# Optimization experiments

Hardware: AMD Instinct MI355X
Metric: run time of the kernel (lower is better)

## Reference

```python
import jax, jax.numpy as jnp
import numpy as np
import math

B, C, A, W, H = 8, 128, 16, 64, 64


def setup_inputs() -> dict:
    key = jax.random.key(0)
    ks = jax.random.split(key, 7)
    s_in = 1.0 / math.sqrt(C)
    return {
        "x": jax.random.normal(ks[0], (B, C, W, H), dtype=jnp.float32),
        "Wq": jax.random.normal(ks[1], (A, C), dtype=jnp.float32) * s_in,
        "bq": jnp.zeros((A,), dtype=jnp.float32),
        "Wk": jax.random.normal(ks[2], (A, C), dtype=jnp.float32) * s_in,
        "bk": jnp.zeros((A,), dtype=jnp.float32),
        "Wv": jax.random.normal(ks[3], (C, C), dtype=jnp.float32) * s_in,
        "bv": jnp.zeros((C,), dtype=jnp.float32),
    }


def reference(x, Wq, bq, Wk, bk, Wv, bv):
    # 1x1 convs == per-pixel linear projections
    q = jnp.einsum('ac,bcwh->bawh', Wq, x) + bq[None, :, None, None]  # [B,A,W,H]
    k = jnp.einsum('ac,bcwh->bawh', Wk, x) + bk[None, :, None, None]  # [B,A,W,H]
    v = jnp.einsum('vc,bcwh->bvwh', Wv, x) + bv[None, :, None, None]  # [B,C,W,H]

    scale = 1.0 / math.sqrt(q.shape[1])
    # full spatial attention: [B, W, H, W, H]
    attn = jnp.einsum('bawh,baWH->bwhWH', q, k)
    b, w, h, _, _ = attn.shape
    attn = jax.nn.softmax(attn.reshape(b, w, h, -1) * scale, axis=-1)
    attn = attn.reshape(b, w, h, w, h)
    out = jnp.einsum('bwhWH,bvWH->bvwh', attn, v)  # [B,C,W,H]
    return out
```

## Files before the change

### kernel.cpp

```cpp
#include <hip/hip_runtime.h>
#include <math.h>

#define BB 8
#define CC 128
#define NN 4096

typedef _Float16 f16;
typedef _Float16 f16x4v __attribute__((ext_vector_type(4)));
typedef _Float16 f16x8 __attribute__((ext_vector_type(8)));
typedef float f32x4v __attribute__((ext_vector_type(4)));
typedef float f32x16 __attribute__((ext_vector_type(16)));

#if __has_builtin(__builtin_amdgcn_exp2f)
#define EXP2(x) __builtin_amdgcn_exp2f(x)
#else
#define EXP2(x) __expf((x)*0.69314718056f)
#endif

#define QSCALE 0.360673760222f
#define SHIFT  5.770780163555f

#define WF_BYTES 65536

__global__ __launch_bounds__(256)
void prep_kernel(const float* __restrict__ Wq, const float* __restrict__ bq,
                 const float* __restrict__ Wk, const float* __restrict__ bk,
                 const float* __restrict__ Wv, const float* __restrict__ bv,
                 f16* __restrict__ Wf, float* __restrict__ biasS)
{
    const int tg = blockIdx.x*256 + threadIdx.x;
    if (tg < 2560) {
        const int mt = tg >> 9, ks = (tg >> 6) & 7, l = tg & 63;
        const int n32 = l & 31, h = l >> 5;
        const int r = mt*32 + n32;
        f16x8 v8;
        #pragma unroll
        for (int i = 0; i < 8; i++) {
            int c = ks*16 + 8*h + i;
            float wv_;
            if (r < 16)      wv_ = QSCALE * Wq[r*CC + c];
            else if (r < 32) wv_ = Wk[(r-16)*CC + c];
            else             wv_ = Wv[(r-32)*CC + c];
            v8[i] = (f16)wv_;
        }
        *(f16x8*)&Wf[(size_t)tg*8] = v8;
    }
    if (blockIdx.x == 0 && threadIdx.x < 160) {
        int r = threadIdx.x;
        biasS[r] = r < 16 ? QSCALE*bq[r] : (r < 32 ? bk[r-16] : bv[r-32]);
    }
}

__global__ __launch_bounds__(256)
void proj_kernel(const float* __restrict__ x, const f16* __restrict__ Wf,
                 const float* __restrict__ biasS,
                 f16* __restrict__ Qt, f16* __restrict__ Kt, f16* __restrict__ Vf)
{
    __shared__ __align__(16) f16 Vl[CC*140];

    const int tid  = threadIdx.x;
    const int lane = tid & 63;
    const int wv   = tid >> 6;
    const int b    = blockIdx.x & 7;
    const int pt   = blockIdx.x >> 3;
    const int n32  = lane & 31;
    const int half = lane >> 5;
    const int p    = pt*128 + wv*32 + n32;

    const float* xp = x + (size_t)b*CC*NN + p;
    f16x8 xf[8];
    #pragma unroll
    for (int ks = 0; ks < 8; ks++) {
        float xv[8];
        #pragma unroll
        for (int i = 0; i < 8; i++)
            xv[i] = __builtin_nontemporal_load(&xp[(size_t)(ks*16 + 8*half + i)*NN]);
        #pragma unroll
        for (int i = 0; i < 8; i++) xf[ks][i] = (f16)xv[i];
    }

    f32x16 acc[5];
    #pragma unroll
    for (int mt = 0; mt < 5; mt++) acc[mt] = (f32x16)0.0f;
    #pragma unroll
    for (int ks = 0; ks < 8; ks++) {
        #pragma unroll
        for (int mt = 0; mt < 5; mt++) {
            f16x8 wfr = *(const f16x8*)&Wf[((size_t)(mt*8 + ks)*64 + lane)*8];
            acc[mt] = __builtin_amdgcn_mfma_f32_32x32x16_f16(wfr, xf[ks], acc[mt], 0, 0, 0);
        }
    }

    #pragma unroll
    for (int mt = 0; mt < 5; mt++) {
        #pragma unroll
        for (int q = 0; q < 4; q++) {
            float4 b4 = *(const float4*)&biasS[mt*32 + q*8 + 4*half];
            acc[mt][q*4+0] += b4.x; acc[mt][q*4+1] += b4.y;
            acc[mt][q*4+2] += b4.z; acc[mt][q*4+3] += b4.w;
        }
    }

    {
        size_t qkoff = ((size_t)b*NN + p)*16;
        f16x4v s0, s1, s2, s3;
        #pragma unroll
        for (int i = 0; i < 4; i++) {
            s0[i] = (f16)acc[0][i];    s1[i] = (f16)acc[0][4+i];
            s2[i] = (f16)acc[0][8+i];  s3[i] = (f16)acc[0][12+i];
        }
        *(f16x4v*)&Qt[qkoff + 4*half]     = s0;
        *(f16x4v*)&Qt[qkoff + 8 + 4*half] = s1;
        *(f16x4v*)&Kt[qkoff + 4*half]     = s2;
        *(f16x4v*)&Kt[qkoff + 8 + 4*half] = s3;
    }

    #pragma unroll
    for (int mt = 1; mt < 5; mt++) {
        #pragma unroll
        for (int g = 0; g < 16; g++) {
            int c = (mt-1)*32 + (g & 3) + 8*(g >> 2) + 4*half;
            Vl[c*140 + wv*32 + n32] = (f16)acc[mt][g];
        }
    }
    __syncthreads();

    #pragma unroll
    for (int pass = 0; pass < 8; pass++) {
        int item = pass*256 + tid;
        int l    = item & 63;
        int f    = (item >> 6) & 15;
        int ktl  = item >> 10;
        int c16  = f >> 2, ct = f & 3;
        int li   = l & 31, h2 = l >> 5;
        const f16* src = &Vl[(ct*32 + li)*140 + ktl*64 + c16*16 + 4*h2];
        f16x4v lo = *(const f16x4v*)&src[0];
        f16x4v hi = *(const f16x4v*)&src[8];
        f16x8 v8;
        #pragma unroll
        for (int i = 0; i < 4; i++) { v8[i] = lo[i]; v8[4+i] = hi[i]; }
        int ktg = pt*2 + ktl;
        *(f16x8*)&Vf[((((size_t)b*64 + ktg)*16 + c16*4 + ct)*64 + l)*8] = v8;
    }
}

__global__ __launch_bounds__(256, 2)
void attn_kernel(const f16* __restrict__ Qt, const f16* __restrict__ Kt,
                 const f16* __restrict__ Vf, float* __restrict__ out)
{
    __shared__ __align__(16) unsigned char lds_raw[53504];

    const int tid  = threadIdx.x;
    const int lane = tid & 63;
    const int w    = tid >> 6;
    const int cp   = w & 1;
    const int kh   = w >> 1;
    const int b    = blockIdx.x & 7;
    const int qt   = blockIdx.x >> 3;
    const int q0   = qt*64;
    const int n32  = lane & 31;
    const int half = lane >> 5;

    const f16* vb = Vf + (size_t)b*64*16*512;
    const f16* kb = Kt + (size_t)b*NN*16;
    const f16x8 qf = *(const f16x8*)&Qt[((size_t)b*NN + q0 + cp*32 + n32)*16 + half*8];

    f32x16 ofA[2], ofB[2];
    #pragma unroll
    for (int c = 0; c < 2; c++) { ofA[c] = (f32x16)0.0f; ofB[c] = (f32x16)0.0f; }
    float ps[4] = {0.f, 0.f, 0.f, 0.f};

    f16x8 kf0 = *(const f16x8*)&kb[((size_t)kh*64 + n32)*16 + half*8];
    f16x8 kf1 = *(const f16x8*)&kb[((size_t)kh*64 + 32 + n32)*16 + half*8];
    f16x8 vpf[8];
    {
        const f16* vt = vb + (size_t)kh*8192;
        #pragma unroll
        for (int kc = 0; kc < 4; kc++)
            #pragma unroll
            for (int j = 0; j < 2; j++)
                vpf[kc*2+j] = *(const f16x8*)&vt[((size_t)(kc*4 + 2*cp + j)*64 + lane)*8];
    }

    f16* Pex = (f16*)lds_raw;
    int pb = 0;

    for (int kt = kh; kt < NN/64; kt += 2) {
        const int ktn = (kt + 2 < NN/64) ? kt + 2 : kt;
        f16x8 kf0n = *(const f16x8*)&kb[((size_t)ktn*64 + n32)*16 + half*8];
        f16x8 kf1n = *(const f16x8*)&kb[((size_t)ktn*64 + 32 + n32)*16 + half*8];

        f16x8 po[4];
        {
            f32x16 St0 = __builtin_amdgcn_mfma_f32_32x32x16_f16(kf0, qf, (f32x16)(-SHIFT), 0, 0, 0);
            f32x16 St1 = __builtin_amdgcn_mfma_f32_32x32x16_f16(kf1, qf, (f32x16)(-SHIFT), 0, 0, 0);
            #pragma unroll
            for (int g = 0; g < 16; g++) {
                float e0 = EXP2(St0[g]); ps[g & 3] += e0; po[(g >> 3)][g & 7]     = (f16)e0;
                float e1 = EXP2(St1[g]); ps[g & 3] += e1; po[2 + (g >> 3)][g & 7] = (f16)e1;
            }
        }

        {
            f16* wr = &Pex[((size_t)(w*2 + pb)*4*64 + lane)*8];
            #pragma unroll
            for (int kc = 0; kc < 4; kc++)
                *(f16x8*)&wr[kc*512] = po[kc];
        }

        #pragma unroll
        for (int kc = 0; kc < 4; kc++) {
            #pragma unroll
            for (int j = 0; j < 2; j++) {
                if (cp == 0)
                    ofA[j] = __builtin_amdgcn_mfma_f32_32x32x16_f16(po[kc], vpf[kc*2+j], ofA[j], 0, 0, 0);
                else
                    ofB[j] = __builtin_amdgcn_mfma_f32_32x32x16_f16(po[kc], vpf[kc*2+j], ofB[j], 0, 0, 0);
            }
        }

        asm volatile("s_waitcnt lgkmcnt(0)\n\ts_barrier" ::: "memory");

        f16x8 pq[4];
        {
            const f16* rd = &Pex[((size_t)((w^1)*2 + pb)*4*64 + lane)*8];
            #pragma unroll
            for (int kc = 0; kc < 4; kc++)
                pq[kc] = *(const f16x8*)&rd[kc*512];
        }

        const f16* vtn = vb + (size_t)ktn*8192;
        #pragma unroll
        for (int kc = 0; kc < 4; kc++) {
            #pragma unroll
            for (int j = 0; j < 2; j++) {
                const int ii = kc*2 + j;
                f16x8 vc = vpf[ii];
                vpf[ii] = *(const f16x8*)&vtn[((size_t)(kc*4 + 2*cp + j)*64 + lane)*8];
                if (cp == 0)
                    ofB[j] = __builtin_amdgcn_mfma_f32_32x32x16_f16(pq[kc], vc, ofB[j], 0, 0, 0);
                else
                    ofA[j] = __builtin_amdgcn_mfma_f32_32x32x16_f16(pq[kc], vc, ofA[j], 0, 0, 0);
            }
        }

        kf0 = kf0n; kf1 = kf1n; pb ^= 1;
    }

    float ls = (ps[0] + ps[1]) + (ps[2] + ps[3]);
    ls += __shfl_xor(ls, 32);

    __syncthreads();
    if (w >= 2) {
        unsigned char* base = lds_raw + (size_t)cp*9216 + (size_t)lane*144;
        #pragma unroll
        for (int a = 0; a < 4; a++) {
            #pragma unroll
            for (int h = 0; h < 2; h++) {
                f16x8 t;
                #pragma unroll
                for (int jj = 0; jj < 8; jj++)
                    t[jj] = (f16)((a < 2 ? ofA[a & 1] : ofB[a & 1])[h*8 + jj]);
                *(f16x8*)(base + a*32 + h*16) = t;
            }
        }
        *(float*)(base + 128) = ls;
    }
    __syncthreads();
    if (w < 2) {
        unsigned char* base = lds_raw + (size_t)cp*9216 + (size_t)lane*144;
        #pragma unroll
        for (int a = 0; a < 4; a++) {
            #pragma unroll
            for (int h = 0; h < 2; h++) {
                f16x8 t = *(const f16x8*)(base + a*32 + h*16);
                #pragma unroll
                for (int jj = 0; jj < 8; jj++) {
                    float v = (float)t[jj];
                    if (a < 2) ofA[a & 1][h*8 + jj] += v;
                    else       ofB[a & 1][h*8 + jj] += v;
                }
            }
        }
        ls += *(const float*)(base + 128);
        float* ls_inv = (float*)(lds_raw + 18432);
        if (lane < 32) ls_inv[cp*32 + n32] = 1.f / ls;
    }
    __syncthreads();

    if (w < 2) {
        const float* ls_inv = (const float*)(lds_raw + 18432);
        float* Tb = (float*)(lds_raw + 18688);
        #pragma unroll
        for (int qts = 0; qts < 2; qts++) {
            #pragma unroll
            for (int j = 0; j < 4; j++) {
                f32x4v iv = *(const f32x4v*)&ls_inv[qts*32 + 8*j + 4*half];
                #pragma unroll
                for (int ctl = 0; ctl < 2; ctl++) {
                    const int c = (2*cp + ctl)*32 + n32;
                    f32x4v o;
                    #pragma unroll
                    for (int e = 0; e < 4; e++)
                        o[e] = (qts ? ofB[ctl] : ofA[ctl])[4*j + e] * iv[e];
                    *(f32x4v*)&Tb[(size_t)c*68 + qts*32 + 8*j + 4*half] = o;
                }
            }
        }
    }
    __syncthreads();
    {
        const float* Tb = (const float*)(lds_raw + 18688);
        #pragma unroll
        for (int it = 0; it < 8; it++) {
            int idx = it*256 + tid;
            int c = idx >> 4, qg = idx & 15;
            f32x4v v = *(const f32x4v*)&Tb[(size_t)c*68 + qg*4];
            __builtin_nontemporal_store(v,
                (f32x4v*)&out[((size_t)b*CC + c)*NN + q0 + qg*4]);
        }
    }
}

extern "C" void kernel_launch(void* const* d_in, const int* in_sizes, int n_in,
                              void* d_out, int out_size, void* d_ws, size_t ws_size,
                              hipStream_t stream) {
    const float* x  = (const float*)d_in[0];
    const float* Wq = (const float*)d_in[1];
    const float* bq = (const float*)d_in[2];
    const float* Wk = (const float*)d_in[3];
    const float* bk = (const float*)d_in[4];
    const float* Wv = (const float*)d_in[5];
    const float* bv = (const float*)d_in[6];
    float* out = (float*)d_out;

    f16* Qw = (f16*)d_ws;
    f16* Kw = Qw + (size_t)BB*NN*16;
    f16* Vw = Kw + (size_t)BB*NN*16;
    unsigned char* tail = (unsigned char*)d_out + (size_t)out_size*4 - WF_BYTES;
    f16*   Wf    = (f16*)tail;
    float* biasS = (float*)(tail + 49152);

    hipLaunchKernelGGL(prep_kernel, dim3(10), dim3(256), 0, stream,
                       Wq, bq, Wk, bk, Wv, bv, Wf, biasS);
    hipLaunchKernelGGL(proj_kernel, dim3(256), dim3(256), 0, stream,
                       x, Wf, biasS, Qw, Kw, Vw);
    hipLaunchKernelGGL(attn_kernel, dim3(512), dim3(256), 0, stream,
                       Qw, Kw, Vw, out);
}
```

Baseline: 136.9 us.

## Double-buffer K/V prefetch two tiles ahead and merge P·V MMAs after barrier

Keeps two register sets of K and V fragments so loads are issued two key tiles ahead, with the loop manually unrolled by two and an explicit epilogue. All P·V MMAs, for both the own and the exchanged probability tile, are moved after the LDS barrier. This hides global-load latency behind more compute at the cost of higher register pressure, which could lower occupancy or cause spills.

```diff
diff --git a/kernel.cpp b/kernel.cpp
--- a/kernel.cpp
+++ b/kernel.cpp
@@ -170,82 +170,115 @@
     for (int c = 0; c < 2; c++) { ofA[c] = (f32x16)0.0f; ofB[c] = (f32x16)0.0f; }
     float ps[4] = {0.f, 0.f, 0.f, 0.f};
 
-    f16x8 kf0 = *(const f16x8*)&kb[((size_t)kh*64 + n32)*16 + half*8];
-    f16x8 kf1 = *(const f16x8*)&kb[((size_t)kh*64 + 32 + n32)*16 + half*8];
-    f16x8 vpf[8];
+    f16x8 kfA0 = *(const f16x8*)&kb[((size_t)kh*64 + n32)*16 + half*8];
+    f16x8 kfA1 = *(const f16x8*)&kb[((size_t)kh*64 + 32 + n32)*16 + half*8];
+    f16x8 kfB0 = *(const f16x8*)&kb[((size_t)(kh+2)*64 + n32)*16 + half*8];
+    f16x8 kfB1 = *(const f16x8*)&kb[((size_t)(kh+2)*64 + 32 + n32)*16 + half*8];
+    f16x8 vpfA[8], vpfB[8];
     {
-        const f16* vt = vb + (size_t)kh*8192;
+        const f16* vtA = vb + (size_t)kh*8192;
+        const f16* vtB = vb + (size_t)(kh+2)*8192;
         #pragma unroll
         for (int kc = 0; kc < 4; kc++)
             #pragma unroll
-            for (int j = 0; j < 2; j++)
-                vpf[kc*2+j] = *(const f16x8*)&vt[((size_t)(kc*4 + 2*cp + j)*64 + lane)*8];
+            for (int j = 0; j < 2; j++) {
+                vpfA[kc*2+j] = *(const f16x8*)&vtA[((size_t)(kc*4 + 2*cp + j)*64 + lane)*8];
+                vpfB[kc*2+j] = *(const f16x8*)&vtB[((size_t)(kc*4 + 2*cp + j)*64 + lane)*8];
+            }
     }
 
     f16* Pex = (f16*)lds_raw;
     int pb = 0;
-
-    for (int kt = kh; kt < NN/64; kt += 2) {
-        const int ktn = (kt + 2 < NN/64) ? kt + 2 : kt;
-        f16x8 kf0n = *(const f16x8*)&kb[((size_t)ktn*64 + n32)*16 + half*8];
-        f16x8 kf1n = *(const f16x8*)&kb[((size_t)ktn*64 + 32 + n32)*16 + half*8];
-
+    const int klast = kh + 62;
+
+#define STEP(KT, KF0, KF1, VPF)                                                       \
+    {                                                                                 \
+        f32x16 St0 = __builtin_amdgcn_mfma_f32_32x32x16_f16(KF0, qf, (f32x16)(-SHIFT), 0, 0, 0); \
+        f32x16 St1 = __builtin_amdgcn_mfma_f32_32x32x16_f16(KF1, qf, (f32x16)(-SHIFT), 0, 0, 0); \
+        int tl = (KT) + 4; if (tl > klast) tl = (KT);                                 \
+        KF0 = *(const f16x8*)&kb[((size_t)tl*64 + n32)*16 + half*8];                  \
+        KF1 = *(const f16x8*)&kb[((size_t)tl*64 + 32 + n32)*16 + half*8];             \
+        f16x8 po[4];                                                                  \
+        _Pragma("unroll")                                                             \
+        for (int g = 0; g < 16; g++) {                                                \
+            float e0 = EXP2(St0[g]); ps[g & 3] += e0; po[(g >> 3)][g & 7]     = (f16)e0; \
+            float e1 = EXP2(St1[g]); ps[g & 3] += e1; po[2 + (g >> 3)][g & 7] = (f16)e1; \
+        }                                                                             \
+        {                                                                             \
+            f16* wr = &Pex[((size_t)(w*2 + pb)*4*64 + lane)*8];                       \
+            _Pragma("unroll")                                                         \
+            for (int kc = 0; kc < 4; kc++) *(f16x8*)&wr[kc*512] = po[kc];             \
+        }                                                                             \
+        asm volatile("s_waitcnt lgkmcnt(0)\n\ts_barrier" ::: "memory");               \
+        f16x8 pq[4];                                                                  \
+        {                                                                             \
+            const f16* rd = &Pex[((size_t)((w^1)*2 + pb)*4*64 + lane)*8];             \
+            _Pragma("unroll")                                                         \
+            for (int kc = 0; kc < 4; kc++) pq[kc] = *(const f16x8*)&rd[kc*512];       \
+        }                                                                             \
+        const f16* vtn = vb + (size_t)tl*8192;                                        \
+        _Pragma("unroll")                                                             \
+        for (int kc = 0; kc < 4; kc++) {                                              \
+            _Pragma("unroll")                                                         \
+            for (int j = 0; j < 2; j++) {                                             \
+                const int ii = kc*2 + j;                                              \
+                f16x8 vc = VPF[ii];                                                   \
+                VPF[ii] = *(const f16x8*)&vtn[((size_t)(kc*4 + 2*cp + j)*64 + lane)*8]; \
+                if (cp == 0) {                                                        \
+                    ofA[j] = __builtin_amdgcn_mfma_f32_32x32x16_f16(po[kc], vc, ofA[j], 0, 0, 0); \
+                    ofB[j] = __builtin_amdgcn_mfma_f32_32x32x16_f16(pq[kc], vc, ofB[j], 0, 0, 0); \
+                } else {                                                              \
+                    ofA[j] = __builtin_amdgcn_mfma_f32_32x32x16_f16(pq[kc], vc, ofA[j], 0, 0, 0); \
+                    ofB[j] = __builtin_amdgcn_mfma_f32_32x32x16_f16(po[kc], vc, ofB[j], 0, 0, 0); \
+                }                                                                     \
+            }                                                                         \
+        }                                                                             \
+        pb ^= 1;                                                                      \
+    }
+
+    for (int it = 0; it < 15; ++it) {
+        const int kt = kh + it*4;
+        STEP(kt,     kfA0, kfA1, vpfA)
+        STEP(kt + 2, kfB0, kfB1, vpfB)
+    }
+    STEP(kh + 60, kfA0, kfA1, vpfA)
+    {
+        f32x16 St0 = __builtin_amdgcn_mfma_f32_32x32x16_f16(kfB0, qf, (f32x16)(-SHIFT), 0, 0, 0);
+        f32x16 St1 = __builtin_amdgcn_mfma_f32_32x32x16_f16(kfB1, qf, (f32x16)(-SHIFT), 0, 0, 0);
         f16x8 po[4];
-        {
-            f32x16 St0 = __builtin_amdgcn_mfma_f32_32x32x16_f16(kf0, qf, (f32x16)(-SHIFT), 0, 0, 0);
-            f32x16 St1 = __builtin_amdgcn_mfma_f32_32x32x16_f16(kf1, qf, (f32x16)(-SHIFT), 0, 0, 0);
-            #pragma unroll
-            for (int g = 0; g < 16; g++) {
-                float e0 = EXP2(St0[g]); ps[g & 3] += e0; po[(g >> 3)][g & 7]     = (f16)e0;
-                float e1 = EXP2(St1[g]); ps[g & 3] += e1; po[2 + (g >> 3)][g & 7] = (f16)e1;
-            }
-        }
-
+        #pragma unroll
+        for (int g = 0; g < 16; g++) {
+            float e0 = EXP2(St0[g]); ps[g & 3] += e0; po[(g >> 3)][g & 7]     = (f16)e0;
+            float e1 = EXP2(St1[g]); ps[g & 3] += e1; po[2 + (g >> 3)][g & 7] = (f16)e1;
+        }
         {
             f16* wr = &Pex[((size_t)(w*2 + pb)*4*64 + lane)*8];
             #pragma unroll
-            for (int kc = 0; kc < 4; kc++)
-                *(f16x8*)&wr[kc*512] = po[kc];
-        }
-
-        #pragma unroll
-        for (int kc = 0; kc < 4; kc++) {
-            #pragma unroll
-            for (int j = 0; j < 2; j++) {
-                if (cp == 0)
-                    ofA[j] = __builtin_amdgcn_mfma_f32_32x32x16_f16(po[kc], vpf[kc*2+j], ofA[j], 0, 0, 0);
-                else
-                    ofB[j] = __builtin_amdgcn_mfma_f32_32x32x16_f16(po[kc], vpf[kc*2+j], ofB[j], 0, 0, 0);
-            }
-        }
-
+            for (int kc = 0; kc < 4; kc++) *(f16x8*)&wr[kc*512] = po[kc];
+        }
         asm volatile("s_waitcnt lgkmcnt(0)\n\ts_barrier" ::: "memory");
-
         f16x8 pq[4];
         {
             const f16* rd = &Pex[((size_t)((w^1)*2 + pb)*4*64 + lane)*8];
             #pragma unroll
-            for (int kc = 0; kc < 4; kc++)
-                pq[kc] = *(const f16x8*)&rd[kc*512];
-        }
-
-        const f16* vtn = vb + (size_t)ktn*8192;
+            for (int kc = 0; kc < 4; kc++) pq[kc] = *(const f16x8*)&rd[kc*512];
+        }
         #pragma unroll
         for (int kc = 0; kc < 4; kc++) {
             #pragma unroll
             for (int j = 0; j < 2; j++) {
-                const int ii = kc*2 + j;
-                f16x8 vc = vpf[ii];
-                vpf[ii] = *(const f16x8*)&vtn[((size_t)(kc*4 + 2*cp + j)*64 + lane)*8];
-                if (cp == 0)
+                f16x8 vc = vpfB[kc*2+j];
+                if (cp == 0) {
+                    ofA[j] = __builtin_amdgcn_mfma_f32_32x32x16_f16(po[kc], vc, ofA[j], 0, 0, 0);
                     ofB[j] = __builtin_amdgcn_mfma_f32_32x32x16_f16(pq[kc], vc, ofB[j], 0, 0, 0);
-                else
+                } else {
                     ofA[j] = __builtin_amdgcn_mfma_f32_32x32x16_f16(pq[kc], vc, ofA[j], 0, 0, 0);
-            }
-        }
-
-        kf0 = kf0n; kf1 = kf1n; pb ^= 1;
-    }
+                    ofB[j] = __builtin_amdgcn_mfma_f32_32x32x16_f16(po[kc], vc, ofB[j], 0, 0, 0);
+                }
+            }
+        }
+    }
+#undef STEP
 
     float ls = (ps[0] + ps[1]) + (ps[2] + ps[3]);
     ls += __shfl_xor(ls, 32);
```

Result: slower. 215.7 us (+57.6%).
